# Kernel optimization log

Hardware: AMD Instinct MI355X
Metric: run time of the kernel (lower is better)

Reference implementation:

```python
import jax, jax.numpy as jnp
import numpy as np

KH, KW = 3, 3
STRIDE = (1, 1)
PAD = ((1, 1), (1, 1))
WEIGHT_BIT = 8


def asym_quant_params(num_bits, smin, smax):
    # ZeroQ asymmetric_linear_quantization_params (signed, integral zero point)
    n = 2.0 ** num_bits - 1.0
    scale = n / jnp.maximum(smax - smin, 1e-8)
    zero_point = jnp.round(scale * smin) + 2.0 ** (num_bits - 1)
    return scale, zero_point


def setup_inputs() -> dict:
    key = jax.random.key(0)
    k1, k2, k3 = jax.random.split(key, 3)
    x = jax.random.normal(k1, (16, 128, 56, 56), dtype=jnp.float32)
    weight = jax.random.normal(k2, (128, 128, 3, 3), dtype=jnp.float32) * 0.05
    bias = jax.random.normal(k3, (128,), dtype=jnp.float32) * 0.1
    return {"x": x, "weight": weight, "bias": bias, "activation_bit": 8}


def reference(x, weight, bias, activation_bit):
    B, C, H, W = x.shape
    Cout = weight.shape[0]

    # nn.functional.unfold(x, 3, stride=1, padding=1).transpose(1, 2)
    # conv_general_dilated_patches emits feature dim ordered (c, kh, kw),
    # matching torch unfold's channel-major layout.
    patches = jax.lax.conv_general_dilated_patches(
        x, filter_shape=(KH, KW), window_strides=STRIDE, padding=PAD)
    _, F, OH, OW = patches.shape          # F = C*KH*KW
    L = OH * OW
    calc_x = patches.reshape(B, F, L).transpose(0, 2, 1)  # [B, L, F]

    # ----- weight quantization: per-output-channel asymmetric int8 -----
    w2 = weight.reshape(Cout, -1)                          # [Cout, F]
    w_min = w2.min(axis=1)
    w_max = w2.max(axis=1)
    scale_w, zp_w = asym_quant_params(WEIGHT_BIT, w_min, w_max)  # [Cout]
    nw = 2.0 ** (WEIGHT_BIT - 1)
    qw = jnp.clip(jnp.round(scale_w[:, None] * w2 - zp_w[:, None]), -nw, nw - 1)

    # ----- activation quantization: per-tensor asymmetric -----
    x_min = calc_x.min()
    x_max = calc_x.max()
    scale_x, zp_x = asym_quant_params(activation_bit, x_min, x_max)
    nx = 2.0 ** (activation_bit - 1)
    qx = jnp.clip(jnp.round(scale_x * calc_x - zp_x), -nx, nx - 1)  # [B, L, F]

    # bias: linear_quantize(bias, scale_w*scale_x, 0)
    qb = jnp.round(scale_w * scale_x * bias)                # [Cout]

    # integer matmul + asymmetric zero-point correction
    # real value r ~= (q + zp) / scale, so
    # x.w*sx*sw = qx.qw + zp_w*sum(qx) + zp_x*sum(qw) + K*zp_w*zp_x
    mult_res = jnp.einsum('blf,of->blo', qx, qw)            # [B, L, Cout]
    K = w2.shape[1]
    res = (mult_res
           + zp_w * qx.sum(-1, keepdims=True)               # [B, L, 1]*[Cout]
           + zp_x * qw.sum(axis=1)                          # [Cout]
           + K * zp_w * zp_x
           + qb)                                            # [B, L, Cout]

    # requantize accumulator to activation_bit bits, then dequantize
    r_min, r_max = res.min(), res.max()
    scale_r, zp_r = asym_quant_params(activation_bit, r_min, r_max)
    nr = 2.0 ** (activation_bit - 1)
    qr = jnp.clip(jnp.round(scale_r * res - zp_r), -nr, nr - 1)
    out = (qr + zp_r) / scale_r / (scale_w * scale_x)       # [B, L, Cout]

    return out.transpose(0, 2, 1)                           # [B, Cout, L]
```

## Files before the change

### kernel.cpp

```cpp
#include <hip/hip_runtime.h>
#include <stdint.h>

#pragma clang fp contract(off)

typedef __attribute__((ext_vector_type(4))) int i32x4;
typedef __attribute__((ext_vector_type(16))) int i32x16;

#define B_    16
#define C_    128
#define HW_   56
#define L_    3136
#define CO_   128
#define F_    1152
#define M_    50176
#define NT_   784

#define OFF_PBMIN 0
#define OFF_PBMAX 4096
#define OFF_PRMIN 8192
#define OFF_PRMAX 12288
#define OFF_SW    16384
#define OFF_ZPW   16896
#define OFF_SXZX  17408
#define OFF_CNT   17536
#define OFF_QS    18048
#define OFF_QW    18560
#define OFF_QX    166016
#define OFF_S     6588544
#define OFF_RES   6789248

__device__ __forceinline__ int read_abit(const int* p) {
    int i = *p;
    if (i > 0 && i < 32) return i;
    float f = __int_as_float(i);
    int fi = (int)f;
    return (fi > 0 && fi < 32) ? fi : 8;
}

__device__ __forceinline__ int swz_tile(int blk) {
    return (blk & 7) * 98 + (blk >> 3);
}

__device__ __forceinline__ void gsync(char* ws) {
    unsigned* base = (unsigned*)(ws + OFF_CNT);
    __syncthreads();
    if (threadIdx.x == 0) {
        __threadfence();
        atomicAdd(&base[(blockIdx.x & 7) * 16], 1u);
    }
    if (threadIdx.x < 8) {
        while (__hip_atomic_load(&base[threadIdx.x * 16],
                                 __ATOMIC_RELAXED, __HIP_MEMORY_SCOPE_AGENT) < 98u)
            __builtin_amdgcn_s_sleep(2);
    }
    __threadfence();
    __syncthreads();
}

__device__ __forceinline__ void block_fminmax(float& mn, float& mx, float* sred) {
    for (int m = 32; m; m >>= 1) {
        mn = fminf(mn, __shfl_xor(mn, m));
        mx = fmaxf(mx, __shfl_xor(mx, m));
    }
    int w = threadIdx.x >> 6;
    if ((threadIdx.x & 63) == 0) { sred[w] = mn; sred[4 + w] = mx; }
    __syncthreads();
    mn = fminf(fminf(sred[0], sred[1]), fminf(sred[2], sred[3]));
    mx = fmaxf(fmaxf(sred[4], sred[5]), fmaxf(sred[6], sred[7]));
    __syncthreads();
}
__device__ __forceinline__ void block_iminmax(int& mn, int& mx, int* ired) {
    for (int m = 32; m; m >>= 1) {
        mn = min(mn, __shfl_xor(mn, m));
        mx = max(mx, __shfl_xor(mx, m));
    }
    int w = threadIdx.x >> 6;
    if ((threadIdx.x & 63) == 0) { ired[w] = mn; ired[4 + w] = mx; }
    __syncthreads();
    mn = min(min(ired[0], ired[1]), min(ired[2], ired[3]));
    mx = max(max(ired[4], ired[5]), max(ired[6], ired[7]));
    __syncthreads();
}
__device__ __forceinline__ int block_isum(int v, int* ired) {
    for (int m = 32; m; m >>= 1) v += __shfl_xor(v, m);
    int w = threadIdx.x >> 6;
    if ((threadIdx.x & 63) == 0) ired[w] = v;
    __syncthreads();
    v = ired[0] + ired[1] + ired[2] + ired[3];
    __syncthreads();
    return v;
}

__global__ __launch_bounds__(256) void kA(const float4* __restrict__ x4,
                                          const float* __restrict__ wgt,
                                          char* __restrict__ ws) {
    __shared__ float sred[8];
    __shared__ int ired[8];
    int blk = blockIdx.x;
    if (blk < NT_) {
        float mn = 0.0f, mx = 0.0f;
        int base = blk * blockDim.x + threadIdx.x;
        int stride = NT_ * 256;
        #pragma unroll
        for (int k = 0; k < 8; ++k) {
            float4 v = x4[base + k * stride];
            mn = fminf(mn, fminf(fminf(v.x, v.y), fminf(v.z, v.w)));
            mx = fmaxf(mx, fmaxf(fmaxf(v.x, v.y), fmaxf(v.z, v.w)));
        }
        block_fminmax(mn, mx, sred);
        if (threadIdx.x == 0) {
            ((float*)(ws + OFF_PBMIN))[blk] = mn;
            ((float*)(ws + OFF_PBMAX))[blk] = mx;
        }
        return;
    }
    int o = blk - NT_;
    const float* wr = wgt + o * F_;
    float mn = 3.4e38f, mx = -3.4e38f;
    for (int f = threadIdx.x; f < F_; f += 256) {
        float v = wr[f];
        mn = fminf(mn, v); mx = fmaxf(mx, v);
    }
    block_fminmax(mn, mx, sred);
    float sw = 255.0f / fmaxf(mx - mn, 1e-8f);
    float zw = rintf(sw * mn) + 128.0f;
    signed char* qw = (signed char*)(ws + OFF_QW);
    int qsum = 0;
    for (int f = threadIdx.x; f < F_; f += 256) {
        float q = fminf(fmaxf(rintf(sw * wr[f] - zw), -128.0f), 127.0f);
        int qi = (int)q;
        qsum += qi;
        int c = f / 9, j = f - c * 9;
        qw[j * 16384 + (c >> 4) * 2048 + (o << 4) + (c & 15)] = (signed char)qi;
    }
    qsum = block_isum(qsum, ired);
    if (threadIdx.x == 0) {
        ((int*)(ws + OFF_QS))[o]  = qsum;
        ((int*)(ws + OFF_ZPW))[o] = (int)zw;
        ((float*)(ws + OFF_SW))[o] = sw;
    }
}

__global__ __launch_bounds__(256) void kP2x(const float* __restrict__ x,
                                            const int* __restrict__ abit_p,
                                            char* __restrict__ ws) {
    __shared__ float sred[8];
    __shared__ int ssum[4][64];
    float mn = 0.0f, mx = 0.0f;
    {
        const float* pbmin = (const float*)(ws + OFF_PBMIN);
        const float* pbmax = (const float*)(ws + OFF_PBMAX);
        for (int i = threadIdx.x; i < NT_; i += 256) {
            mn = fminf(mn, pbmin[i]);
            mx = fmaxf(mx, pbmax[i]);
        }
        block_fminmax(mn, mx, sred);
    }
    int abit = read_abit(abit_p);
    float nlv = (float)((1 << abit) - 1);
    float sx = nlv / fmaxf(mx - mn, 1e-8f);
    float zx = rintf(sx * mn) + (float)(1 << (abit - 1));
    if (threadIdx.x == 0 && blockIdx.x == 0) {
        ((float*)(ws + OFF_SXZX))[0] = sx;
        ((float*)(ws + OFF_SXZX))[1] = zx;
    }
    int nx = 1 << (abit - 1);
    float lo = -(float)nx, hif = (float)(nx - 1);
    signed char* qxt = (signed char*)(ws + OFF_QX);
    int gid = swz_tile(blockIdx.x);
    int b = gid / 49, lcq = gid - b * 49;
    int l0 = lcq * 64;
    int t = threadIdx.x, lane = t & 63, cgp = t >> 6;
    int l = l0 + lane;
    const float* xb = x + ((size_t)b * C_) * L_ + l;
    int4* dst = (int4*)(qxt + ((size_t)(b * L_ + l)) * 128);
    int psum = 0;
    #pragma unroll
    for (int ii = 0; ii < 2; ++ii) {
        int c16 = (cgp + 4 * ii) * 16;
        int wds[4];
        #pragma unroll
        for (int k = 0; k < 4; ++k) {
            int wv = 0;
            #pragma unroll
            for (int e = 0; e < 4; ++e) {
                int c = c16 + 4 * k + e;
                float v = xb[(size_t)c * L_];
                int qi = (int)fminf(fmaxf(rintf(sx * v - zx), lo), hif);
                psum += qi;
                wv |= (qi & 255) << (8 * e);
            }
            wds[k] = wv;
        }
        int4 vv; vv.x = wds[0]; vv.y = wds[1]; vv.z = wds[2]; vv.w = wds[3];
        dst[c16 >> 4] = vv;
    }
    ssum[cgp][lane] = psum;
    __syncthreads();
    if (cgp == 0) {
        int* S = (int*)(ws + OFF_S);
        S[b * L_ + l] = ssum[0][lane] + ssum[1][lane] + ssum[2][lane] + ssum[3][lane];
    }
}

template <bool WRITE_RES>
__device__ __forceinline__ void dev_p3(char* __restrict__ ws, char* pool, int* ired,
                                       const float* __restrict__ bias,
                                       int abit, float sx, float zx,
                                       i32x16& acc0, i32x16& acc1) {
    signed char* As = (signed char*)pool;
    signed char* Bs = (signed char*)(pool + 8192);
    int* S_s = (int*)(pool + 24576);
    int* sq  = (int*)(pool + 25504);
    const signed char* qxt = (const signed char*)(ws + OFF_QX);
    const signed char* qw  = (const signed char*)(ws + OFF_QW);
    const int* Sg  = (const int*)(ws + OFF_S);
    const int* zpw = (const int*)(ws + OFF_ZPW);

    int t = threadIdx.x;
    int mg = swz_tile(blockIdx.x) * 64;
    int b = mg / L_, l0 = mg - b * L_;
    int prow0 = l0 / HW_;
    int nx = 1 << (abit - 1);
    int q0 = min(max(-(int)zx, -nx), nx - 1);
    int pw = (q0 & 255) * 0x01010101;
    int4 pad4; pad4.x = pw; pad4.y = pw; pad4.z = pw; pad4.w = pw;
    int padS = C_ * q0;
    const signed char* qxtb = qxt + (size_t)b * L_ * 128;
    const int* Sb = Sg + b * L_;

    int chA = t & 7, rowA0 = t >> 3, rowA1 = rowA0 + 32;
    int li0 = l0 + rowA0, li1 = l0 + rowA1;
    int oh0 = li0 / HW_, ow0 = li0 - oh0 * HW_;
    int oh1 = li1 / HW_, ow1 = li1 - oh1 * HW_;

    int4 a0, a1, br0, br1, br2, br3;
    #define P3_LOAD_A(J) do {                                                          \
        int kh = (J) / 3 - 1, kw = (J) % 3 - 1;                                        \
        int ih = oh0 + kh, iw = ow0 + kw;                                              \
        a0 = ((unsigned)ih < HW_ && (unsigned)iw < HW_)                                \
             ? *(const int4*)(qxtb + ((ih * HW_ + iw) << 7) + (chA << 4)) : pad4;      \
        ih = oh1 + kh; iw = ow1 + kw;                                                  \
        a1 = ((unsigned)ih < HW_ && (unsigned)iw < HW_)                                \
             ? *(const int4*)(qxtb + ((ih * HW_ + iw) << 7) + (chA << 4)) : pad4;      \
    } while (0)
    #define P3_LOAD_B(J) do {                                                          \
        const int4* src = (const int4*)(qw + (J) * 16384);                             \
        br0 = src[t]; br1 = src[256 + t]; br2 = src[512 + t]; br3 = src[768 + t];      \
    } while (0)

    P3_LOAD_A(0); P3_LOAD_B(0);
    if (t < 232) {
        int ri = t / 58, c1 = t - ri * 58;
        int ih = prow0 - 1 + ri, iw = c1 - 1;
        S_s[t] = ((unsigned)ih < HW_ && (unsigned)iw < HW_) ? Sb[ih * HW_ + iw] : padS;
    }
    __syncthreads();
    if (t < 64) {
        int l = l0 + t;
        int oh = l / HW_, ow = l - oh * HW_;
        int ri = oh - prow0 + 1, ci = ow + 1;
        int s = 0;
        #pragma unroll
        for (int dr = -1; dr <= 1; ++dr)
            #pragma unroll
            for (int dc = -1; dc <= 1; ++dc)
                s += S_s[(ri + dr) * 58 + ci + dc];
        sq[t] = s;
    }

    int lane = t & 63, w = t >> 6;
    int wm = (w >> 1) << 5, wn = (w & 1) << 6;
    int r = lane & 31, hi = lane >> 5;
    #pragma unroll
    for (int i = 0; i < 16; ++i) { acc0[i] = 0; acc1[i] = 0; }

    #pragma unroll
    for (int j = 0; j < 9; ++j) {
        if (j > 0) __syncthreads();
        *(int4*)&As[(rowA0 << 7) + ((chA ^ (rowA0 & 7)) << 4)] = a0;
        *(int4*)&As[(rowA1 << 7) + ((chA ^ (rowA1 & 7)) << 4)] = a1;
        {
            int4* d = (int4*)Bs;
            d[t] = br0; d[256 + t] = br1; d[512 + t] = br2; d[768 + t] = br3;
        }
        if (j < 8) { P3_LOAD_A(j + 1); P3_LOAD_B(j + 1); }
        __syncthreads();
        i32x4 af[4], bf0[4], bf1[4];
        #pragma unroll
        for (int kk = 0; kk < 4; ++kk) {
            int ch2 = kk * 2 + hi, row = wm + r;
            af[kk]  = *(const i32x4*)&As[(row << 7) + ((ch2 ^ (row & 7)) << 4)];
            bf0[kk] = *(const i32x4*)&Bs[ch2 * 2048 + ((wn + r) << 4)];
            bf1[kk] = *(const i32x4*)&Bs[ch2 * 2048 + ((wn + 32 + r) << 4)];
        }
        #pragma unroll
        for (int kk = 0; kk < 4; ++kk) {
            acc0 = __builtin_amdgcn_mfma_i32_32x32x32_i8(af[kk], bf0[kk], acc0, 0, 0, 0);
            acc1 = __builtin_amdgcn_mfma_i32_32x32x32_i8(af[kk], bf1[kk], acc1, 0, 0, 0);
        }
    }
    #undef P3_LOAD_A
    #undef P3_LOAD_B

    int o0 = wn + r, o1 = wn + 32 + r;
    const int* qs = (const int*)(ws + OFF_QS);
    const float* swp = (const float*)(ws + OFF_SW);
    int zxi = (int)zx;
    int zw0 = zpw[o0], zw1 = zpw[o1];
    int c0 = zxi * qs[o0] + F_ * zw0 * zxi + (int)rintf(swp[o0] * sx * bias[o0]);
    int c1 = zxi * qs[o1] + F_ * zw1 * zxi + (int)rintf(swp[o1] * sx * bias[o1]);
    int lmin = INT32_MAX, lmax = INT32_MIN;
    int* resp = (int*)(ws + OFF_RES);
    #pragma unroll
    for (int g = 0; g < 16; ++g) {
        int row = wm + (g & 3) + ((g >> 2) << 3) + (hi << 2);
        int s = sq[row];
        int v0 = acc0[g] + zw0 * s + c0;
        int v1 = acc1[g] + zw1 * s + c1;
        acc0[g] = v0; acc1[g] = v1;
        lmin = min(lmin, min(v0, v1));
        lmax = max(lmax, max(v0, v1));
        if (WRITE_RES) {
            int m = mg + row;
            resp[m * CO_ + o0] = v0;
            resp[m * CO_ + o1] = v1;
        }
    }
    block_iminmax(lmin, lmax, ired);
    if (t == 0) {
        ((int*)(ws + OFF_PRMIN))[blockIdx.x] = lmin;
        ((int*)(ws + OFF_PRMAX))[blockIdx.x] = lmax;
    }
    __syncthreads();
}

__device__ __forceinline__ void dev_reduce_pr(const char* ws, int* ired,
                                              int& rmin, int& rmax) {
    const int* prmin = (const int*)(ws + OFF_PRMIN);
    const int* prmax = (const int*)(ws + OFF_PRMAX);
    int mn = INT32_MAX, mx = INT32_MIN;
    for (int i = threadIdx.x; i < NT_; i += 256) {
        mn = min(mn, prmin[i]);
        mx = max(mx, prmax[i]);
    }
    block_iminmax(mn, mx, ired);
    rmin = mn; rmax = mx;
}

__global__ __launch_bounds__(256, 4) void kCoop(const float* __restrict__ bias,
                                                const int* __restrict__ abit_p,
                                                char* __restrict__ ws,
                                                float* __restrict__ out) {
    __shared__ __align__(16) char pool[33280];
    __shared__ int ired[8];

    float sx = ((const float*)(ws + OFF_SXZX))[0];
    float zx = ((const float*)(ws + OFF_SXZX))[1];
    int abit = read_abit(abit_p);

    i32x16 acc0, acc1;
    dev_p3<false>(ws, pool, ired, bias, abit, sx, zx, acc0, acc1);
    gsync(ws);

    int rmin, rmax;
    dev_reduce_pr(ws, ired, rmin, rmax);

    const float* swp = (const float*)(ws + OFF_SW);
    int t = threadIdx.x;
    int mg = swz_tile(blockIdx.x) * 64;
    int b = mg / L_, l0 = mg - b * L_;
    int lane = t & 63, w = t >> 6;
    int wm = (w >> 1) << 5, wn = (w & 1) << 6;
    int r = lane & 31, hi = lane >> 5;
    int o0 = wn + r, o1 = wn + 32 + r;
    int nx = 1 << (abit - 1);
    float nlev = (float)((1 << abit) - 1);
    float sr = nlev / fmaxf((float)rmax - (float)rmin, 1e-8f);
    float zr = rintf(sr * (float)rmin) + (float)nx;
    float lo = -(float)nx, hiq = (float)(nx - 1);
    float swsx0 = swp[o0] * sx, swsx1 = swp[o1] * sx;
    float* tile = (float*)pool;
    #pragma unroll
    for (int g = 0; g < 16; ++g) {
        int row = wm + (g & 3) + ((g >> 2) << 3) + (hi << 2);
        float qa = fminf(fmaxf(rintf(sr * (float)acc0[g] - zr), lo), hiq);
        float qb = fminf(fmaxf(rintf(sr * (float)acc1[g] - zr), lo), hiq);
        tile[row * 129 + o0] = ((qa + zr) / sr) / swsx0;
        tile[row * 129 + o1] = ((qb + zr) / sr) / swsx1;
    }
    __syncthreads();
    #pragma unroll
    for (int i = 0; i < 8; ++i) {
        int o = (t >> 4) + i * 16;
        int l4 = (t & 15) * 4;
        float4 f;
        #pragma unroll
        for (int jj = 0; jj < 4; ++jj)
            ((float*)&f)[jj] = tile[(l4 + jj) * 129 + o];
        *(float4*)(out + ((size_t)(b * CO_ + o)) * L_ + l0 + l4) = f;
    }
}

__global__ __launch_bounds__(256, 4) void fbGEMM(const float* __restrict__ bias,
                                                 const int* __restrict__ abit_p,
                                                 char* __restrict__ ws) {
    __shared__ __align__(16) char pool[25760];
    __shared__ int ired[8];
    float sx = ((const float*)(ws + OFF_SXZX))[0];
    float zx = ((const float*)(ws + OFF_SXZX))[1];
    int abit = read_abit(abit_p);
    i32x16 acc0, acc1;
    dev_p3<true>(ws, pool, ired, bias, abit, sx, zx, acc0, acc1);
}

__global__ __launch_bounds__(256) void fbDEQ(const int* __restrict__ abit_p,
                                             char* __restrict__ ws,
                                             float* __restrict__ out) {
    __shared__ int tile[64 * 65];
    __shared__ int ired[8];
    float sxv = ((const float*)(ws + OFF_SXZX))[0];
    int abit = read_abit(abit_p);
    float nlv = (float)((1 << abit) - 1);
    int rmin, rmax;
    dev_reduce_pr(ws, ired, rmin, rmax);

    const int* res = (const int*)(ws + OFF_RES);
    const float* scale_w = (const float*)(ws + OFF_SW);
    int t = threadIdx.x;
    int bid = blockIdx.x;
    int lcq = bid % 49; int tmp2 = bid / 49; int ocq = tmp2 & 1; int b = tmp2 >> 1;
    int l0 = lcq * 64, o0 = ocq * 64;

    const int* resb = res + ((size_t)(b * L_ + l0)) * CO_ + o0;
    #pragma unroll
    for (int i = 0; i < 4; ++i) {
        int lr = (t >> 4) + i * 16;
        int oc4 = (t & 15) * 4;
        int4 v = *(const int4*)(resb + lr * CO_ + oc4);
        int* d = &tile[lr * 65 + oc4];
        d[0] = v.x; d[1] = v.y; d[2] = v.z; d[3] = v.w;
    }
    int nxq = 1 << (abit - 1);
    float sr = nlv / fmaxf((float)rmax - (float)rmin, 1e-8f);
    float zr = rintf(sr * (float)rmin) + (float)nxq;
    float lo = -(float)nxq, hiq = (float)(nxq - 1);
    __syncthreads();
    #pragma unroll
    for (int i = 0; i < 4; ++i) {
        int o = (t >> 4) + i * 16;
        int l4 = (t & 15) * 4;
        float swsx = scale_w[o0 + o] * sxv;
        float4 f;
        #pragma unroll
        for (int jj = 0; jj < 4; ++jj) {
            int rv = tile[(l4 + jj) * 65 + o];
            float q = fminf(fmaxf(rintf(sr * (float)rv - zr), lo), hiq);
            ((float*)&f)[jj] = ((q + zr) / sr) / swsx;
        }
        *(float4*)(out + ((size_t)(b * CO_ + o0 + o)) * L_ + l0 + l4) = f;
    }
}


extern "C" void kernel_launch(void* const* d_in, const int* in_sizes, int n_in,
                              void* d_out, int out_size, void* d_ws, size_t ws_size,
                              hipStream_t stream) {
    const float* x      = (const float*)d_in[0];
    const float* weight = (const float*)d_in[1];
    const float* bias   = (const float*)d_in[2];
    const int*   abit   = (const int*)d_in[3];
    float* out = (float*)d_out;
    char* ws = (char*)d_ws;

    int dev = 0;
    hipGetDevice(&dev);
    int ncu = 0;
    hipDeviceGetAttribute(&ncu, hipDeviceAttributeMultiprocessorCount, dev);
    int nb = 0;
    hipOccupancyMaxActiveBlocksPerMultiprocessor(&nb, (const void*)kCoop, 256, 0);

    kA<<<NT_ + CO_, 256, 0, stream>>>((const float4*)x, weight, ws);
    kP2x<<<NT_, 256, 0, stream>>>(x, abit, ws);

    if (nb > 0 && (long)nb * (long)ncu >= NT_) {
        hipMemsetAsync(ws + OFF_CNT, 0, 512, stream);
        kCoop<<<NT_, 256, 0, stream>>>(bias, abit, ws, out);
    } else {
        fbGEMM<<<NT_, 256, 0, stream>>>(bias, abit, ws);
        fbDEQ<<<1568, 256, 0, stream>>>(abit, ws, out);
    }
}
```

Measured before the change: 54.02 us.

## Load A fragments straight to registers and double-buffer B in LDS

```diff
diff --git a/kernel.cpp b/kernel.cpp
--- a/kernel.cpp
+++ b/kernel.cpp
@@ -208,10 +208,10 @@
                                        const float* __restrict__ bias,
                                        int abit, float sx, float zx,
                                        i32x16& acc0, i32x16& acc1) {
-    signed char* As = (signed char*)pool;
-    signed char* Bs = (signed char*)(pool + 8192);
-    int* S_s = (int*)(pool + 24576);
-    int* sq  = (int*)(pool + 25504);
+    signed char* Bs0 = (signed char*)pool;
+    signed char* Bs1 = (signed char*)(pool + 16384);
+    int* S_s = (int*)(pool + 16384);
+    int* sq  = (int*)(pool + 32768);
     const signed char* qxt = (const signed char*)(ws + OFF_QX);
     const signed char* qw  = (const signed char*)(ws + OFF_QW);
     const int* Sg  = (const int*)(ws + OFF_S);
@@ -224,32 +224,34 @@
     int nx = 1 << (abit - 1);
     int q0 = min(max(-(int)zx, -nx), nx - 1);
     int pw = (q0 & 255) * 0x01010101;
-    int4 pad4; pad4.x = pw; pad4.y = pw; pad4.z = pw; pad4.w = pw;
+    i32x4 padv; padv[0] = pw; padv[1] = pw; padv[2] = pw; padv[3] = pw;
     int padS = C_ * q0;
     const signed char* qxtb = qxt + (size_t)b * L_ * 128;
     const int* Sb = Sg + b * L_;
 
-    int chA = t & 7, rowA0 = t >> 3, rowA1 = rowA0 + 32;
-    int li0 = l0 + rowA0, li1 = l0 + rowA1;
-    int oh0 = li0 / HW_, ow0 = li0 - oh0 * HW_;
-    int oh1 = li1 / HW_, ow1 = li1 - oh1 * HW_;
-
-    int4 a0, a1, br0, br1, br2, br3;
-    #define P3_LOAD_A(J) do {                                                          \
-        int kh = (J) / 3 - 1, kw = (J) % 3 - 1;                                        \
-        int ih = oh0 + kh, iw = ow0 + kw;                                              \
-        a0 = ((unsigned)ih < HW_ && (unsigned)iw < HW_)                                \
-             ? *(const int4*)(qxtb + ((ih * HW_ + iw) << 7) + (chA << 4)) : pad4;      \
-        ih = oh1 + kh; iw = ow1 + kw;                                                  \
-        a1 = ((unsigned)ih < HW_ && (unsigned)iw < HW_)                                \
-             ? *(const int4*)(qxtb + ((ih * HW_ + iw) << 7) + (chA << 4)) : pad4;      \
-    } while (0)
+    int lane = t & 63, w = t >> 6;
+    int wm = (w >> 1) << 5, wn = (w & 1) << 6;
+    int r = lane & 31, hi = lane >> 5;
+
+    int lrow = l0 + wm + r;
+    int oh = lrow / HW_, ow = lrow - oh * HW_;
+
+    int4 br0, br1, br2, br3;
     #define P3_LOAD_B(J) do {                                                          \
         const int4* src = (const int4*)(qw + (J) * 16384);                             \
         br0 = src[t]; br1 = src[256 + t]; br2 = src[512 + t]; br3 = src[768 + t];      \
     } while (0)
-
-    P3_LOAD_A(0); P3_LOAD_B(0);
+    #define P3_LOAD_AF(J, DST) do {                                                    \
+        int kh = (J) / 3 - 1, kw = (J) % 3 - 1;                                        \
+        int ih = oh + kh, iw = ow + kw;                                                \
+        bool vld = ((unsigned)ih < HW_) && ((unsigned)iw < HW_);                       \
+        const signed char* ap = qxtb + (((ih * HW_ + iw) << 7) & 0x7FFFFFFF);          \
+        _Pragma("unroll")                                                              \
+        for (int kk = 0; kk < 4; ++kk)                                                 \
+            DST[kk] = vld ? *(const i32x4*)(ap + (((kk << 1) + hi) << 4)) : padv;      \
+    } while (0)
+
+    P3_LOAD_B(0);
     if (t < 232) {
         int ri = t / 58, c1 = t - ri * 58;
         int ih = prow0 - 1 + ri, iw = c1 - 1;
@@ -258,8 +260,8 @@
     __syncthreads();
     if (t < 64) {
         int l = l0 + t;
-        int oh = l / HW_, ow = l - oh * HW_;
-        int ri = oh - prow0 + 1, ci = ow + 1;
+        int oh2 = l / HW_, ow2 = l - oh2 * HW_;
+        int ri = oh2 - prow0 + 1, ci = ow2 + 1;
         int s = 0;
         #pragma unroll
         for (int dr = -1; dr <= 1; ++dr)
@@ -268,40 +270,45 @@
                 s += S_s[(ri + dr) * 58 + ci + dc];
         sq[t] = s;
     }
-
-    int lane = t & 63, w = t >> 6;
-    int wm = (w >> 1) << 5, wn = (w & 1) << 6;
-    int r = lane & 31, hi = lane >> 5;
+    {
+        int4* d = (int4*)Bs0;
+        d[t] = br0; d[256 + t] = br1; d[512 + t] = br2; d[768 + t] = br3;
+        P3_LOAD_B(1);
+    }
+    i32x4 afc[4], afn[4];
+    P3_LOAD_AF(0, afc);
+    __syncthreads();
+
     #pragma unroll
     for (int i = 0; i < 16; ++i) { acc0[i] = 0; acc1[i] = 0; }
 
     #pragma unroll
     for (int j = 0; j < 9; ++j) {
-        if (j > 0) __syncthreads();
-        *(int4*)&As[(rowA0 << 7) + ((chA ^ (rowA0 & 7)) << 4)] = a0;
-        *(int4*)&As[(rowA1 << 7) + ((chA ^ (rowA1 & 7)) << 4)] = a1;
-        {
-            int4* d = (int4*)Bs;
+        if (j < 8) {
+            int4* d = (int4*)(((j + 1) & 1) ? Bs1 : Bs0);
             d[t] = br0; d[256 + t] = br1; d[512 + t] = br2; d[768 + t] = br3;
-        }
-        if (j < 8) { P3_LOAD_A(j + 1); P3_LOAD_B(j + 1); }
+            if (j < 7) P3_LOAD_B(j + 2);
+        }
+        const signed char* Bc = (j & 1) ? Bs1 : Bs0;
+        i32x4 bf0[4], bf1[4];
+        #pragma unroll
+        for (int kk = 0; kk < 4; ++kk) {
+            int ch2 = (kk << 1) + hi;
+            bf0[kk] = *(const i32x4*)&Bc[ch2 * 2048 + ((wn + r) << 4)];
+            bf1[kk] = *(const i32x4*)&Bc[ch2 * 2048 + ((wn + 32 + r) << 4)];
+        }
+        if (j < 8) P3_LOAD_AF(j + 1, afn);
+        #pragma unroll
+        for (int kk = 0; kk < 4; ++kk) {
+            acc0 = __builtin_amdgcn_mfma_i32_32x32x32_i8(afc[kk], bf0[kk], acc0, 0, 0, 0);
+            acc1 = __builtin_amdgcn_mfma_i32_32x32x32_i8(afc[kk], bf1[kk], acc1, 0, 0, 0);
+        }
+        #pragma unroll
+        for (int kk = 0; kk < 4; ++kk) afc[kk] = afn[kk];
         __syncthreads();
-        i32x4 af[4], bf0[4], bf1[4];
-        #pragma unroll
-        for (int kk = 0; kk < 4; ++kk) {
-            int ch2 = kk * 2 + hi, row = wm + r;
-            af[kk]  = *(const i32x4*)&As[(row << 7) + ((ch2 ^ (row & 7)) << 4)];
-            bf0[kk] = *(const i32x4*)&Bs[ch2 * 2048 + ((wn + r) << 4)];
-            bf1[kk] = *(const i32x4*)&Bs[ch2 * 2048 + ((wn + 32 + r) << 4)];
-        }
-        #pragma unroll
-        for (int kk = 0; kk < 4; ++kk) {
-            acc0 = __builtin_amdgcn_mfma_i32_32x32x32_i8(af[kk], bf0[kk], acc0, 0, 0, 0);
-            acc1 = __builtin_amdgcn_mfma_i32_32x32x32_i8(af[kk], bf1[kk], acc1, 0, 0, 0);
-        }
-    }
-    #undef P3_LOAD_A
+    }
     #undef P3_LOAD_B
+    #undef P3_LOAD_AF
 
     int o0 = wn + r, o1 = wn + 32 + r;
     const int* qs = (const int*)(ws + OFF_QS);
@@ -405,7 +412,7 @@
 __global__ __launch_bounds__(256, 4) void fbGEMM(const float* __restrict__ bias,
                                                  const int* __restrict__ abit_p,
                                                  char* __restrict__ ws) {
-    __shared__ __align__(16) char pool[25760];
+    __shared__ __align__(16) char pool[33280];
     __shared__ int ired[8];
     float sx = ((const float*)(ws + OFF_SXZX))[0];
     float zx = ((const float*)(ws + OFF_SXZX))[1];
```

New measurement: 65.35 us. 1.21x slower.
